# Optimization experiments

Measured on AMD Instinct MI355X. Metric: run time of the kernel, lower is better.

The kernel has to match this reference:

```python
import jax, jax.numpy as jnp
import numpy as np

B, E, H = 128, 512, 1024
NEG = -1000000.0


def setup_inputs() -> dict:
    key = jax.random.key(0)
    ks = jax.random.split(key, 10)
    inv = 1.0 / np.sqrt(H)
    return {
        "query": jax.random.normal(ks[0], (B, H), jnp.float32),
        "keys": jax.random.normal(ks[1], (B, E, H), jnp.float32),
        "entity_size": jax.random.randint(ks[2], (B,), 0, E + 1, jnp.int32),
        "mention_score": jax.random.normal(ks[3], (B,), jnp.float32),
        # scorer params (torch Linear(2H->H) then Linear(H->1)), stored transposed
        "W1": jax.random.normal(ks[4], (2 * H, H), jnp.float32) * inv,
        "b1": jnp.zeros((H,), jnp.float32),
        "W2": jax.random.normal(ks[5], (H, 1), jnp.float32) * inv,
        "b2": jnp.zeros((1,), jnp.float32),
        "null_address": jax.random.normal(ks[6], (H,), jnp.float32) * inv,
        "new_address": jax.random.normal(ks[7], (H,), jnp.float32) * inv,
    }


def reference(query, keys, entity_size, mention_score, W1, b1, W2, b2, null_address, new_address):
    b, e, h = keys.shape
    # prepend null address, append new address -> [B, E+2, H]
    null = jnp.broadcast_to(null_address, (b, 1, h))
    new = jnp.broadcast_to(new_address, (b, 1, h))
    keys_full = jnp.concatenate([null, keys, new], axis=1)
    q = jnp.broadcast_to(query[:, None, :], (b, e + 2, h))
    qk = jnp.concatenate([q, keys_full], axis=-1)  # [B, E+2, 2H]
    hid = jax.nn.gelu(jnp.einsum("bsd,dh->bsh", qk, W1) + b1, approximate=False)
    scores = (jnp.einsum("bsh,ho->bso", hid, W2) + b2)[..., 0]  # [B, E+2]
    # mention score with sign flip on the null slot (column 0)
    inv_mask = jnp.ones((e + 2,), scores.dtype).at[0].set(-1.0)
    scores = scores + mention_score[:, None] * inv_mask[None, :]
    # mask out slots entity_size[b]+1 .. E (exclusive of the final 'new' slot)
    idx = jnp.arange(e + 2)
    mask = jnp.where((idx[None, :] >= entity_size[:, None] + 1) & (idx[None, :] <= e), NEG, 0.0).astype(scores.dtype)
    return scores + mask
```

## Files before the change

kernel.cpp:

```cpp
#include <hip/hip_runtime.h>
#include <hip/hip_bf16.h>

#define B_ 128
#define E_ 512
#define H_ 1024
#define S_ 514
#define NEGV -1000000.0f

typedef __attribute__((ext_vector_type(8))) short bf16x8;
typedef __attribute__((ext_vector_type(4))) short s16x4;
typedef __attribute__((ext_vector_type(4))) float f32x4;

typedef __attribute__((address_space(1))) const void* gptr_t;
typedef __attribute__((address_space(3))) void* lptr_t;

__device__ __forceinline__ short f2bf(float f) {
  unsigned u = __builtin_bit_cast(unsigned, f);
  return (short)((u + 0x8000u) >> 16);
}

__device__ __forceinline__ float gelu_f(float x) {
  return 0.5f * x * (1.0f + erff(x * 0.7071067811865475f));
}

__global__ void init_q1(const float* __restrict__ b1, float* __restrict__ Q1,
                        float* __restrict__ N1, float* __restrict__ A1) {
  int b = blockIdx.x;
  int t = threadIdx.x;
  if (b < B_) {
    f32x4 v = *(const f32x4*)(b1 + t * 4);
    *(f32x4*)(Q1 + (size_t)b * H_ + t * 4) = v;
  } else if (b == B_) {
    *(f32x4*)(N1 + t * 4) = (f32x4){0.f, 0.f, 0.f, 0.f};
  } else {
    *(f32x4*)(A1 + t * 4) = (f32x4){0.f, 0.f, 0.f, 0.f};
  }
}

#define RPB 8
__global__ void prep2(const float* __restrict__ query, const float* __restrict__ W1,
                      const float* __restrict__ nulla, const float* __restrict__ newa,
                      float* __restrict__ Q1, float* __restrict__ N1, float* __restrict__ A1) {
  int bid = blockIdx.x;
  int rg = bid >> 4;
  int dc = bid & 15;
  int t = threadIdx.x;
  bool special = (rg == 16);
  int woff = special ? H_ : 0;

  __shared__ float vec[RPB][64];
  {
    int r = t >> 6, dd = t & 63;
    #pragma unroll
    for (int rr = 0; rr < 2; ++rr) {
      int row = r + rr * 4;
      float v = 0.f;
      if (!special) v = query[(size_t)(rg * RPB + row) * H_ + dc * 64 + dd];
      else if (row == 0) v = nulla[dc * 64 + dd];
      else if (row == 1) v = newa[dc * 64 + dd];
      vec[row][dd] = v;
    }
  }
  __syncthreads();

  const float* wp = W1 + (size_t)(woff + dc * 64) * H_ + t * 4;
  f32x4 acc[RPB];
  #pragma unroll
  for (int r = 0; r < RPB; ++r) acc[r] = (f32x4){0.f, 0.f, 0.f, 0.f};

  #pragma unroll 4
  for (int dd = 0; dd < 64; ++dd) {
    f32x4 w = *(const f32x4*)(wp + (size_t)dd * H_);
    #pragma unroll
    for (int r = 0; r < RPB; ++r) {
      float v = vec[r][dd];
      acc[r][0] += v * w[0]; acc[r][1] += v * w[1];
      acc[r][2] += v * w[2]; acc[r][3] += v * w[3];
    }
  }

  if (!special) {
    #pragma unroll
    for (int r = 0; r < RPB; ++r) {
      float* dst = Q1 + (size_t)(rg * RPB + r) * H_ + t * 4;
      atomicAdd(dst + 0, acc[r][0]); atomicAdd(dst + 1, acc[r][1]);
      atomicAdd(dst + 2, acc[r][2]); atomicAdd(dst + 3, acc[r][3]);
    }
  } else {
    float* d0 = N1 + t * 4;
    atomicAdd(d0 + 0, acc[0][0]); atomicAdd(d0 + 1, acc[0][1]);
    atomicAdd(d0 + 2, acc[0][2]); atomicAdd(d0 + 3, acc[0][3]);
    float* d1 = A1 + t * 4;
    atomicAdd(d1 + 0, acc[1][0]); atomicAdd(d1 + 1, acc[1][1]);
    atomicAdd(d1 + 2, acc[1][2]); atomicAdd(d1 + 3, acc[1][3]);
  }
}

__global__ void transpose_w1k(const float* __restrict__ W1, short* __restrict__ w1kT) {
  __shared__ float tb[64][65];
  int k0 = (blockIdx.x & 15) * 64;
  int n0 = (blockIdx.x >> 4) * 64;
  int x = threadIdx.x & 63;
  int ty = threadIdx.x >> 6;
  #pragma unroll
  for (int i = 0; i < 16; ++i) {
    int row = i * 4 + ty;
    tb[row][x] = W1[(size_t)(H_ + k0 + row) * H_ + n0 + x];
  }
  __syncthreads();
  #pragma unroll
  for (int i = 0; i < 16; ++i) {
    int row = i * 4 + ty;
    w1kT[(size_t)(n0 + row) * H_ + k0 + x] = f2bf(tb[x][row]);
  }
}

__global__ void finalize_base(const int* __restrict__ es, const float* __restrict__ mention,
                              const float* __restrict__ W2, const float* __restrict__ b2,
                              const float* __restrict__ Q1, const float* __restrict__ N1,
                              const float* __restrict__ A1, float* __restrict__ scores) {
  int b = blockIdx.x;
  int t = threadIdx.x;
  float b2v = b2[0], mv = mention[b];
  int esz = es[b];
  for (int s = t; s < S_; s += 256) {
    float base = b2v + (s == 0 ? -mv : mv);
    if (s >= esz + 1 && s <= E_) base += NEGV;
    scores[b * S_ + s] = base;
  }
  float sum0 = 0.f, sum1 = 0.f;
  for (int h = t; h < H_; h += 256) {
    float q = Q1[b * H_ + h], w = W2[h];
    sum0 += gelu_f(q + N1[h]) * w;
    sum1 += gelu_f(q + A1[h]) * w;
  }
  #pragma unroll
  for (int m = 32; m > 0; m >>= 1) { sum0 += __shfl_xor(sum0, m); sum1 += __shfl_xor(sum1, m); }
  __shared__ float red0[4], red1[4];
  int lanei = t & 63, wdi = t >> 6;
  if (lanei == 0) { red0[wdi] = sum0; red1[wdi] = sum1; }
  __syncthreads();
  if (t == 0) {
    scores[b * S_ + 0]      += red0[0] + red0[1] + red0[2] + red0[3];
    scores[b * S_ + S_ - 1] += red1[0] + red1[1] + red1[2] + red1[3];
  }
}

#define GBM 128
#define GBN 128
#define GBK 64

__global__ __launch_bounds__(256, 2) void gemm_fused(
    const float* __restrict__ keys, const short* __restrict__ Bm,
    const float* __restrict__ Q1, const float* __restrict__ W2,
    float* __restrict__ scores) {
  __shared__ short As[GBM * GBK];
  __shared__ short Bs[GBN * GBK];

  int bid = blockIdx.x;
  int cpx = gridDim.x >> 3;
  bid = (bid & 7) * cpx + (bid >> 3);
  int tileM = bid >> 3;
  int tileN = bid & 7;
  int row0 = tileM * GBM;
  int col0 = tileN * GBN;

  int t = threadIdx.x;
  int lane = t & 63;
  int wid = t >> 6;
  int wr = wid >> 1, wc = wid & 1;
  int l15 = lane & 15, lHi = lane >> 4;

  int asr = t >> 4;
  int asc = (t & 15) * 4;
  const float* aBase = keys + (size_t)(row0 + asr) * H_ + asc;
  char* aWr = (char*)As + asr * 128 + ((((t & 15) * 8)) ^ ((asr & 7) << 4));

  int srcRow = lane >> 3;
  int srcColE = ((lane & 7) ^ (lane >> 3)) << 3;
  const short* bSrc = Bm + (size_t)(col0 + wid * 32 + srcRow) * H_ + srcColE;
  short* bDst = Bs + (wid * 4) * 512;

  f32x4 aReg[8];
  f32x4 acc[4][4];
  #pragma unroll
  for (int m = 0; m < 4; ++m)
    #pragma unroll
    for (int n = 0; n < 4; ++n) acc[m][n] = (f32x4){0.f, 0.f, 0.f, 0.f};

  #pragma unroll
  for (int p = 0; p < 8; ++p) aReg[p] = *(const f32x4*)(aBase + (size_t)p * 16 * H_);

  int swz = (l15 & 7) << 4;
  const char* aRd = (const char*)As + (wr * 64 + l15) * 128;
  const char* bRd = (const char*)Bs + (wc * 64 + l15) * 128;

  for (int k0 = 0; k0 < H_; k0 += GBK) {
    __syncthreads();
    #pragma unroll
    for (int p = 0; p < 8; ++p) {
      s16x4 v;
      #pragma unroll
      for (int j = 0; j < 4; ++j) v[j] = f2bf(aReg[p][j]);
      *(s16x4*)(aWr + p * 2048) = v;
    }
    #pragma unroll
    for (int i = 0; i < 4; ++i)
      __builtin_amdgcn_global_load_lds((gptr_t)(bSrc + (size_t)i * 8 * H_ + k0),
                                       (lptr_t)(bDst + i * 512), 16, 0, 0);
    __syncthreads();
    if (k0 + GBK < H_) {
      #pragma unroll
      for (int p = 0; p < 8; ++p)
        aReg[p] = *(const f32x4*)(aBase + (size_t)p * 16 * H_ + k0 + GBK);
    }
    #pragma unroll
    for (int kk = 0; kk < 2; ++kk) {
      bf16x8 af[4], bv[4];
      #pragma unroll
      for (int m = 0; m < 4; ++m)
        af[m] = *(const bf16x8*)(aRd + m * 2048 + (((kk << 6) | (lHi << 4)) ^ swz));
      #pragma unroll
      for (int n = 0; n < 4; ++n)
        bv[n] = *(const bf16x8*)(bRd + n * 2048 + (((kk << 6) | (lHi << 4)) ^ swz));
      #pragma unroll
      for (int m = 0; m < 4; ++m)
        #pragma unroll
        for (int n = 0; n < 4; ++n)
          acc[m][n] = __builtin_amdgcn_mfma_f32_16x16x32_bf16(af[m], bv[n], acc[m][n], 0, 0, 0);
    }
  }

  int bIdx = row0 >> 9;
  float q1v[4], w2v[4];
  #pragma unroll
  for (int n = 0; n < 4; ++n) {
    int col = col0 + wc * 64 + n * 16 + l15;
    q1v[n] = Q1[bIdx * H_ + col];
    w2v[n] = W2[col];
  }
  #pragma unroll
  for (int m = 0; m < 4; ++m) {
    float part[4] = {0.f, 0.f, 0.f, 0.f};
    #pragma unroll
    for (int n = 0; n < 4; ++n)
      #pragma unroll
      for (int i = 0; i < 4; ++i)
        part[i] += gelu_f(acc[m][n][i] + q1v[n]) * w2v[n];
    #pragma unroll
    for (int i = 0; i < 4; ++i) {
      float v = part[i];
      v += __shfl_xor(v, 1);
      v += __shfl_xor(v, 2);
      v += __shfl_xor(v, 4);
      v += __shfl_xor(v, 8);
      if (l15 == 0) {
        int row = row0 + wr * 64 + m * 16 + lHi * 4 + i;
        int s = (row & 511) + 1;
        atomicAdd(&scores[bIdx * S_ + s], v);
      }
    }
  }
}

extern "C" void kernel_launch(void* const* d_in, const int* in_sizes, int n_in,
                              void* d_out, int out_size, void* d_ws, size_t ws_size,
                              hipStream_t stream) {
  const float* query   = (const float*)d_in[0];
  const float* keys    = (const float*)d_in[1];
  const int*   esz     = (const int*)d_in[2];
  const float* mention = (const float*)d_in[3];
  const float* W1      = (const float*)d_in[4];
  const float* b1      = (const float*)d_in[5];
  const float* W2      = (const float*)d_in[6];
  const float* b2      = (const float*)d_in[7];
  const float* nulla   = (const float*)d_in[8];
  const float* newa    = (const float*)d_in[9];
  float* scores = (float*)d_out;

  const size_t w1kTBytes = (size_t)H_ * H_ * 2;
  short* w1kT = (short*)d_ws;
  float* Q1   = (float*)((char*)d_ws + w1kTBytes);
  float* N1   = Q1 + (size_t)B_ * H_;
  float* A1   = N1 + H_;

  init_q1<<<130, 256, 0, stream>>>(b1, Q1, N1, A1);
  prep2<<<272, 256, 0, stream>>>(query, W1, nulla, newa, Q1, N1, A1);
  transpose_w1k<<<256, 256, 0, stream>>>(W1, w1kT);
  finalize_base<<<B_, 256, 0, stream>>>(esz, mention, W2, b2, Q1, N1, A1, scores);
  gemm_fused<<<4096, 256, 0, stream>>>(keys, w1kT, Q1, W2, scores);
}
```

Baseline: 643.8 us.

## Double-buffer B tile in LDS and widen A staging to 16-byte writes

Double-buffers the B tile in shared memory so the async global-to-LDS load for the next K step is issued before the current step's MFMAs and overlaps with them. A-tile staging is remapped so each thread converts 8 consecutive floats and writes one 16-byte bf16 vector per row group instead of 8-byte pieces, with the swizzle adjusted to match. Launch bounds rise from 2 to 3 blocks per SM, which tightens the register budget and could cause spills. Extra LDS use (about 48KB per block) may limit how many blocks are actually resident.

Result: slower. 657.8 us (+2.2%).

```diff
diff --git a/kernel.cpp b/kernel.cpp
--- a/kernel.cpp
+++ b/kernel.cpp
@@ -150,12 +150,12 @@
 #define GBN 128
 #define GBK 64
 
-__global__ __launch_bounds__(256, 2) void gemm_fused(
+__global__ __launch_bounds__(256, 3) void gemm_fused(
     const float* __restrict__ keys, const short* __restrict__ Bm,
     const float* __restrict__ Q1, const float* __restrict__ W2,
     float* __restrict__ scores) {
   __shared__ short As[GBM * GBK];
-  __shared__ short Bs[GBN * GBK];
+  __shared__ short Bs[2][GBN * GBK];
 
   int bid = blockIdx.x;
   int cpx = gridDim.x >> 3;
@@ -171,17 +171,17 @@
   int wr = wid >> 1, wc = wid & 1;
   int l15 = lane & 15, lHi = lane >> 4;
 
-  int asr = t >> 4;
-  int asc = (t & 15) * 4;
-  const float* aBase = keys + (size_t)(row0 + asr) * H_ + asc;
-  char* aWr = (char*)As + asr * 128 + ((((t & 15) * 8)) ^ ((asr & 7) << 4));
+  int uc = t & 7;
+  int rBase = t >> 3;
+  const float* aBase = keys + (size_t)(row0 + rBase) * H_ + uc * 8;
+  char* aWr = (char*)As + rBase * 128 + ((uc ^ (rBase & 7)) << 4);
 
   int srcRow = lane >> 3;
   int srcColE = ((lane & 7) ^ (lane >> 3)) << 3;
   const short* bSrc = Bm + (size_t)(col0 + wid * 32 + srcRow) * H_ + srcColE;
-  short* bDst = Bs + (wid * 4) * 512;
-
-  f32x4 aReg[8];
+  int bDstOff = (wid * 4) * 512;
+
+  f32x4 aReg[4][2];
   f32x4 acc[4][4];
   #pragma unroll
   for (int m = 0; m < 4; ++m)
@@ -189,31 +189,45 @@
     for (int n = 0; n < 4; ++n) acc[m][n] = (f32x4){0.f, 0.f, 0.f, 0.f};
 
   #pragma unroll
-  for (int p = 0; p < 8; ++p) aReg[p] = *(const f32x4*)(aBase + (size_t)p * 16 * H_);
+  for (int p = 0; p < 4; ++p) {
+    aReg[p][0] = *(const f32x4*)(aBase + (size_t)p * 32 * H_);
+    aReg[p][1] = *(const f32x4*)(aBase + (size_t)p * 32 * H_ + 4);
+  }
+  #pragma unroll
+  for (int i = 0; i < 4; ++i)
+    __builtin_amdgcn_global_load_lds((gptr_t)(bSrc + (size_t)i * 8 * H_),
+                                     (lptr_t)(&Bs[0][bDstOff + i * 512]), 16, 0, 0);
 
   int swz = (l15 & 7) << 4;
   const char* aRd = (const char*)As + (wr * 64 + l15) * 128;
-  const char* bRd = (const char*)Bs + (wc * 64 + l15) * 128;
-
-  for (int k0 = 0; k0 < H_; k0 += GBK) {
+  const char* bRd0 = (const char*)&Bs[0][0] + (wc * 64 + l15) * 128;
+  const char* bRd1 = (const char*)&Bs[1][0] + (wc * 64 + l15) * 128;
+
+  for (int ti = 0; ti < H_ / GBK; ++ti) {
+    int cur = ti & 1;
     __syncthreads();
     #pragma unroll
-    for (int p = 0; p < 8; ++p) {
-      s16x4 v;
-      #pragma unroll
-      for (int j = 0; j < 4; ++j) v[j] = f2bf(aReg[p][j]);
-      *(s16x4*)(aWr + p * 2048) = v;
-    }
-    #pragma unroll
-    for (int i = 0; i < 4; ++i)
-      __builtin_amdgcn_global_load_lds((gptr_t)(bSrc + (size_t)i * 8 * H_ + k0),
-                                       (lptr_t)(bDst + i * 512), 16, 0, 0);
+    for (int p = 0; p < 4; ++p) {
+      bf16x8 v;
+      #pragma unroll
+      for (int j = 0; j < 4; ++j) { v[j] = f2bf(aReg[p][0][j]); v[4 + j] = f2bf(aReg[p][1][j]); }
+      *(bf16x8*)(aWr + p * 4096) = v;
+    }
     __syncthreads();
-    if (k0 + GBK < H_) {
-      #pragma unroll
-      for (int p = 0; p < 8; ++p)
-        aReg[p] = *(const f32x4*)(aBase + (size_t)p * 16 * H_ + k0 + GBK);
-    }
+    int k1 = (ti + 1) * GBK;
+    if (k1 < H_) {
+      short* bDstN = (cur ? &Bs[0][0] : &Bs[1][0]) + bDstOff;
+      #pragma unroll
+      for (int i = 0; i < 4; ++i)
+        __builtin_amdgcn_global_load_lds((gptr_t)(bSrc + (size_t)i * 8 * H_ + k1),
+                                         (lptr_t)(bDstN + i * 512), 16, 0, 0);
+      #pragma unroll
+      for (int p = 0; p < 4; ++p) {
+        aReg[p][0] = *(const f32x4*)(aBase + (size_t)p * 32 * H_ + k1);
+        aReg[p][1] = *(const f32x4*)(aBase + (size_t)p * 32 * H_ + k1 + 4);
+      }
+    }
+    const char* bRdCur = cur ? bRd1 : bRd0;
     #pragma unroll
     for (int kk = 0; kk < 2; ++kk) {
       bf16x8 af[4], bv[4];
@@ -222,7 +236,7 @@
         af[m] = *(const bf16x8*)(aRd + m * 2048 + (((kk << 6) | (lHi << 4)) ^ swz));
       #pragma unroll
       for (int n = 0; n < 4; ++n)
-        bv[n] = *(const bf16x8*)(bRd + n * 2048 + (((kk << 6) | (lHi << 4)) ^ swz));
+        bv[n] = *(const bf16x8*)(bRdCur + n * 2048 + (((kk << 6) | (lHi << 4)) ^ swz));
       #pragma unroll
       for (int m = 0; m < 4; ++m)
         #pragma unroll
```
